# Performance work log

Measured on AMD Instinct MI355X. Metric: run time of the kernel, lower is better.

## Reference

```python
import jax, jax.numpy as jnp
import numpy as np

E = 300      # embedding size
H = 150      # LSTM units per direction
D = 300      # biLSTM output dim (2*H)
VOCAB = 200000
SEQ = 2048


def _lstm(x, W, U, b, reverse=False):
    # x: [S, E] -> hidden states [S, H]; keras gate order i,f,g(c),o
    xp = x @ W + b  # [S, 4H]
    h0 = jnp.zeros((H,), x.dtype)
    c0 = jnp.zeros((H,), x.dtype)

    def step(carry, xt):
        h, c = carry
        z = xt + h @ U
        i = jax.nn.sigmoid(z[:H])
        f = jax.nn.sigmoid(z[H:2 * H])
        g = jnp.tanh(z[2 * H:3 * H])
        o = jax.nn.sigmoid(z[3 * H:])
        c = f * c + i * g
        h = o * jnp.tanh(c)
        return (h, c), h

    _, hs = jax.lax.scan(step, (h0, c0), xp, reverse=reverse)
    return hs


def _primary_attention(out, hidden_states, syn_emb):
    # out: [S, D] projected hidden states; syn_emb: [S, 4, E]
    att = jnp.exp(jnp.einsum('sd,skd->sk', out, syn_emb))      # [S, 4]
    m = jnp.einsum('sk,skd->sd', att, syn_emb)                 # [S, E]
    return jnp.concatenate([hidden_states, m], axis=-1)        # [S, D+E]


def _secondary_attention(h, w, b):
    coeff = jnp.exp(jnp.tanh(h @ w + b))                       # [S, 1]
    return jnp.sum(coeff * h, axis=0)                          # [D+E]


def setup_inputs() -> dict:
    key = jax.random.key(0)
    ks = jax.random.split(key, 20)
    s = 0.05
    inp = {
        'sentence': jax.random.randint(ks[0], (SEQ,), 0, VOCAB),
        'embedding_matrix': jax.random.normal(ks[1], (VOCAB, E), jnp.float32),
        'synonym_indices': jax.random.randint(ks[2], (VOCAB, 4), 0, VOCAB),
        # forward LSTM
        'Wf': jax.random.normal(ks[3], (E, 4 * H), jnp.float32) * s,
        'Uf': jax.random.normal(ks[4], (H, 4 * H), jnp.float32) * s,
        'bf': jnp.zeros((4 * H,), jnp.float32),
        # backward LSTM
        'Wb': jax.random.normal(ks[5], (E, 4 * H), jnp.float32) * s,
        'Ub': jax.random.normal(ks[6], (H, 4 * H), jnp.float32) * s,
        'bb': jnp.zeros((4 * H,), jnp.float32),
        # primary attention dense layers (D -> D)
        'W_pe': jax.random.normal(ks[7], (D, D), jnp.float32) * s,
        'b_pe': jnp.zeros((D,), jnp.float32),
        'W_ps': jax.random.normal(ks[8], (D, D), jnp.float32) * s,
        'b_ps': jnp.zeros((D,), jnp.float32),
        # secondary attention dense layers (D+E -> 1, tanh)
        'w_se': jax.random.normal(ks[9], (D + E, 1), jnp.float32) * s,
        'b_se': jnp.zeros((1,), jnp.float32),
        'w_ss': jax.random.normal(ks[10], (D + E, 1), jnp.float32) * s,
        'b_ss': jnp.zeros((1,), jnp.float32),
        # output layers
        'W_eo': jax.random.normal(ks[11], (D + E, 8), jnp.float32) * s,
        'b_eo': jnp.zeros((8,), jnp.float32),
        'W_so': jax.random.normal(ks[12], (D + E, 1), jnp.float32) * s,
        'b_so': jnp.zeros((1,), jnp.float32),
    }
    return inp


def reference(sentence, embedding_matrix, synonym_indices,
              Wf, Uf, bf, Wb, Ub, bb,
              W_pe, b_pe, W_ps, b_ps,
              w_se, b_se, w_ss, b_ss,
              W_eo, b_eo, W_so, b_so):
    embeddings = embedding_matrix[sentence]                    # [S, E]
    h_fwd = _lstm(embeddings, Wf, Uf, bf, reverse=False)       # [S, H]
    h_bwd = _lstm(embeddings, Wb, Ub, bb, reverse=True)        # [S, H]
    hidden_states = jnp.concatenate([h_fwd, h_bwd], axis=-1)   # [S, D]

    syn_emb = embedding_matrix[synonym_indices[sentence]]      # [S, 4, E]

    out_s = hidden_states @ W_ps + b_ps
    h_hats = _primary_attention(out_s, hidden_states, syn_emb)  # [S, D+E]
    out_e = hidden_states @ W_pe + b_pe
    h_bars = _primary_attention(out_e, hidden_states, syn_emb)  # [S, D+E]

    H_HAT = _secondary_attention(h_hats, w_ss, b_ss)[None, :]   # [1, D+E]
    H_BAR = _secondary_attention(h_bars, w_se, b_se)[None, :]   # [1, D+E]

    sentiment_logits = H_HAT @ W_so + b_so                      # [1, 1]
    emotion_logits = H_BAR @ W_eo + b_eo                        # [1, 8]
    return (emotion_logits, sentiment_logits)
```

## Files before the change

kernel.cpp:

```cpp
#include <hip/hip_runtime.h>
#include <hip/hip_bf16.h>

#define SEQ  2048
#define EDIM 300
#define HDIM 150
#define FH   600
#define DDIM 300
#define DE   600

__device__ __forceinline__ float frcp_(float x) { return __builtin_amdgcn_rcpf(x); }
__device__ __forceinline__ float sigm_(float x) { return frcp_(1.f + __expf(-x)); }
__device__ __forceinline__ float tanh_(float x) { return 1.f - 2.f * frcp_(1.f + __expf(2.f * x)); }

__device__ __forceinline__ float wave_red(float v) {
#pragma unroll
    for (int off = 32; off; off >>= 1) v += __shfl_down(v, off, 64);
    return v;
}

__device__ __forceinline__ float rl_(float v, int l) {
    return __uint_as_float((unsigned)__builtin_amdgcn_readlane(__float_as_uint(v), l));
}

__global__ __launch_bounds__(256) void k_xp(
    const int* __restrict__ sent, const float* __restrict__ emb,
    const float* __restrict__ Wf, const float* __restrict__ bfv,
    const float* __restrict__ Wb, const float* __restrict__ bbv,
    float* __restrict__ xpf, float* __restrict__ xpb)
{
    __shared__ float xs[16][EDIM];
    const int tid = threadIdx.x;
    const int t0  = blockIdx.x * 16;

    for (int i = tid; i < 16 * EDIM; i += 256) {
        int r = i / EDIM, e = i - r * EDIM;
        int row = sent[t0 + r];
        xs[r][e] = emb[(size_t)row * EDIM + e];
    }
    __syncthreads();

    float acc[5][16];
#pragma unroll
    for (int c = 0; c < 5; c++)
#pragma unroll
        for (int r = 0; r < 16; r++) acc[c][r] = 0.f;

    const float* wp[5];
    bool val[5];
#pragma unroll
    for (int c = 0; c < 5; c++) {
        int j = tid + 256 * c;
        val[c] = (j < 1200);
        wp[c] = (j < 600) ? (Wf + j) : (Wb + (j < 1200 ? j - 600 : 0));
    }

    for (int e = 0; e < EDIM; e++) {
        float xr[16];
#pragma unroll
        for (int r = 0; r < 16; r++) xr[r] = xs[r][e];
#pragma unroll
        for (int c = 0; c < 5; c++) {
            if (val[c]) {
                float w = wp[c][(size_t)e * FH];
#pragma unroll
                for (int r = 0; r < 16; r++) acc[c][r] += xr[r] * w;
            }
        }
    }

#pragma unroll
    for (int c = 0; c < 5; c++) {
        int j = tid + 256 * c;
        if (j < 1200) {
            bool isF = (j < 600);
            int jj = isF ? j : j - 600;
            float bias = isF ? bfv[jj] : bbv[jj];
            float* dst = isF ? xpf : xpb;
#pragma unroll
            for (int r = 0; r < 16; r++)
                dst[(size_t)(t0 + r) * FH + jj] = acc[c][r] + bias;
        }
    }
}

__global__ __launch_bounds__(512, 2) void k_lstm(
    const float* __restrict__ Uf, const float* __restrict__ Ub,
    const float* __restrict__ xpf, const float* __restrict__ xpb,
    float* __restrict__ hs)
{
    const int dir = blockIdx.x;
    const float* __restrict__ U  = dir ? Ub : Uf;
    const float* __restrict__ xp = dir ? xpb : xpf;

    __shared__ float zpart[2][4][FH];

    const int tid  = threadIdx.x;
    const int lane = tid & 63;
    const int wv   = tid >> 6;
    const int kg   = wv & 3;
    const int cg   = wv >> 2;
    const int kw0  = kg * 38;

    const bool has5 = (lane < 44);
    int col[5];
#pragma unroll
    for (int g = 0; g < 5; g++) {
        int c = 300 * cg + 64 * g + lane;
        col[g] = (g == 4 && !has5) ? (300 * cg + 299) : c;
    }

    float Ur[5][38];
#pragma unroll
    for (int kk = 0; kk < 38; kk++) {
        const int k   = kw0 + kk;
        const bool kv = (k < HDIM);
        const float* row = U + (size_t)(kv ? k : 0) * FH;
        const float m = kv ? 1.f : 0.f;
#pragma unroll
        for (int g = 0; g < 5; g++)
            Ur[g][kk] = m * row[col[g]];
    }

    const int j  = kw0 + lane;
    const bool gv = (lane < 38) && (j < HDIM);
    float hreg = 0.f, creg = 0.f;

    float xq0 = 0.f, xq1 = 0.f, xq2 = 0.f, xq3 = 0.f;
    if (gv) {
        const float* xrow = xp + (size_t)(dir ? (SEQ - 1) : 0) * FH;
        xq0 = xrow[j];
        xq1 = xrow[HDIM + j];
        xq2 = xrow[2 * HDIM + j];
        xq3 = xrow[3 * HDIM + j];
    }

    for (int step = 0; step < SEQ; step++) {
        const int t = dir ? (SEQ - 1 - step) : step;
        const int p = step & 1;

        float s0 = 0.f, s1 = 0.f, s2 = 0.f, s3 = 0.f, s4 = 0.f;
#pragma unroll
        for (int kk = 0; kk < 38; kk++) {
            const float hk = rl_(hreg, kk);
            s0 = fmaf(hk, Ur[0][kk], s0);
            s1 = fmaf(hk, Ur[1][kk], s1);
            s2 = fmaf(hk, Ur[2][kk], s2);
            s3 = fmaf(hk, Ur[3][kk], s3);
            s4 = fmaf(hk, Ur[4][kk], s4);
        }
        zpart[p][kg][col[0]] = s0;
        zpart[p][kg][col[1]] = s1;
        zpart[p][kg][col[2]] = s2;
        zpart[p][kg][col[3]] = s3;
        if (has5) zpart[p][kg][col[4]] = s4;

        asm volatile("s_waitcnt lgkmcnt(0)" ::: "memory");
        __builtin_amdgcn_sched_barrier(0);
        __builtin_amdgcn_s_barrier();
        __builtin_amdgcn_sched_barrier(0);

        if (gv) {
            float z0 = xq0, z1 = xq1, z2 = xq2, z3 = xq3;
#pragma unroll
            for (int k4 = 0; k4 < 4; k4++) {
                z0 += zpart[p][k4][j];
                z1 += zpart[p][k4][HDIM + j];
                z2 += zpart[p][k4][2 * HDIM + j];
                z3 += zpart[p][k4][3 * HDIM + j];
            }

            if (step + 1 < SEQ) {
                const int tn = dir ? (SEQ - 2 - step) : (step + 1);
                const float* xrow = xp + (size_t)tn * FH;
                xq0 = xrow[j];
                xq1 = xrow[HDIM + j];
                xq2 = xrow[2 * HDIM + j];
                xq3 = xrow[3 * HDIM + j];
            }

            const float ig = sigm_(z0);
            const float fg = sigm_(z1);
            const float gg = tanh_(z2);
            const float og = sigm_(z3);
            creg = fg * creg + ig * gg;
            hreg = og * tanh_(creg);

            if (cg == 0)
                hs[(size_t)t * DDIM + dir * HDIM + j] = hreg;
        }
    }
}

__global__ __launch_bounds__(256) void k_out(
    const float* __restrict__ hs,
    const float* __restrict__ Wpe, const float* __restrict__ bpe,
    const float* __restrict__ Wps, const float* __restrict__ bps,
    float* __restrict__ oe, float* __restrict__ os)
{
    __shared__ float xs[16 * DDIM];
    const int tid = threadIdx.x;
    const int t0  = blockIdx.x * 16;

    for (int i = tid; i < 16 * DDIM; i += 256) xs[i] = hs[(size_t)t0 * DDIM + i];
    __syncthreads();

    float acc[3][16];
#pragma unroll
    for (int c = 0; c < 3; c++)
#pragma unroll
        for (int r = 0; r < 16; r++) acc[c][r] = 0.f;

    const float* wp[3];
    bool val[3];
#pragma unroll
    for (int c = 0; c < 3; c++) {
        int j = tid + 256 * c;
        val[c] = (j < 600);
        wp[c] = (j < 300) ? (Wpe + j) : (Wps + (j < 600 ? j - 300 : 0));
    }

    for (int e = 0; e < DDIM; e++) {
        float xr[16];
#pragma unroll
        for (int r = 0; r < 16; r++) xr[r] = xs[r * DDIM + e];
#pragma unroll
        for (int c = 0; c < 3; c++) {
            if (val[c]) {
                float w = wp[c][(size_t)e * DDIM];
#pragma unroll
                for (int r = 0; r < 16; r++) acc[c][r] += xr[r] * w;
            }
        }
    }

#pragma unroll
    for (int c = 0; c < 3; c++) {
        int j = tid + 256 * c;
        if (j < 600) {
            bool isE = (j < 300);
            int jj = isE ? j : j - 300;
            float bias = isE ? bpe[jj] : bps[jj];
            float* dst = isE ? oe : os;
#pragma unroll
            for (int r = 0; r < 16; r++)
                dst[(size_t)(t0 + r) * DDIM + jj] = acc[c][r] + bias;
        }
    }
}

__global__ __launch_bounds__(256) void k_attn(
    const int* __restrict__ sent, const int* __restrict__ syn,
    const float* __restrict__ emb,
    const float* __restrict__ hs, const float* __restrict__ oeA, const float* __restrict__ osA,
    const float* __restrict__ w_se, const float* __restrict__ b_se,
    const float* __restrict__ w_ss, const float* __restrict__ b_ss,
    float* __restrict__ accHat, float* __restrict__ accBar)
{
    __shared__ float Loe[DDIM], Los[DDIM], Lh[DDIM];
    __shared__ float Lsyn[4][EDIM];
    __shared__ float Lme[EDIM], Lms[EDIM];
    __shared__ float Lred[4][8];
    __shared__ float Latt[8];
    __shared__ float Lco[2];

    const int tid = threadIdx.x;
    const int wv = tid >> 6, lane = tid & 63;
    float aH[3] = {0.f, 0.f, 0.f}, aB[3] = {0.f, 0.f, 0.f};

    for (int i8 = 0; i8 < 8; i8++) {
        const int s = blockIdx.x * 8 + i8;
        for (int i = tid; i < DDIM; i += 256) {
            Loe[i] = oeA[(size_t)s * DDIM + i];
            Los[i] = osA[(size_t)s * DDIM + i];
            Lh[i]  = hs [(size_t)s * DDIM + i];
        }
        const int sid = sent[s];
        for (int i = tid; i < 4 * EDIM; i += 256) {
            int k4 = i / EDIM, e = i - k4 * EDIM;
            int row = syn[sid * 4 + k4];
            Lsyn[k4][e] = emb[(size_t)row * EDIM + e];
        }
        __syncthreads();

        float p[8];
#pragma unroll
        for (int q = 0; q < 8; q++) p[q] = 0.f;
        for (int d = tid; d < EDIM; d += 256) {
            float voe = Loe[d], vos = Los[d];
#pragma unroll
            for (int k4 = 0; k4 < 4; k4++) {
                float sv = Lsyn[k4][d];
                p[k4]     += voe * sv;
                p[4 + k4] += vos * sv;
            }
        }
#pragma unroll
        for (int q = 0; q < 8; q++) {
            float r = wave_red(p[q]);
            if (lane == 0) Lred[wv][q] = r;
        }
        __syncthreads();
        if (tid < 8)
            Latt[tid] = __expf(Lred[0][tid] + Lred[1][tid] + Lred[2][tid] + Lred[3][tid]);
        __syncthreads();

        for (int d = tid; d < EDIM; d += 256) {
            float me = 0.f, ms = 0.f;
#pragma unroll
            for (int k4 = 0; k4 < 4; k4++) {
                float sv = Lsyn[k4][d];
                me += Latt[k4] * sv;
                ms += Latt[4 + k4] * sv;
            }
            Lme[d] = me; Lms[d] = ms;
        }
        __syncthreads();

        float pe = 0.f, ps = 0.f;
        for (int d = tid; d < DE; d += 256) {
            float ve = (d < DDIM) ? Lh[d] : Lme[d - DDIM];
            float vs = (d < DDIM) ? Lh[d] : Lms[d - DDIM];
            pe += ve * w_se[d];
            ps += vs * w_ss[d];
        }
        pe = wave_red(pe); ps = wave_red(ps);
        if (lane == 0) { Lred[wv][0] = pe; Lred[wv][1] = ps; }
        __syncthreads();
        if (tid == 0) {
            float de_ = Lred[0][0] + Lred[1][0] + Lred[2][0] + Lred[3][0];
            float ds_ = Lred[0][1] + Lred[1][1] + Lred[2][1] + Lred[3][1];
            Lco[0] = __expf(tanh_(de_ + b_se[0]));
            Lco[1] = __expf(tanh_(ds_ + b_ss[0]));
        }
        __syncthreads();
        float ce = Lco[0], cs = Lco[1];
#pragma unroll
        for (int cc = 0; cc < 3; cc++) {
            int d = tid + 256 * cc;
            if (d < DE) {
                float ve = (d < DDIM) ? Lh[d] : Lme[d - DDIM];
                float vs = (d < DDIM) ? Lh[d] : Lms[d - DDIM];
                aB[cc] += ce * ve;
                aH[cc] += cs * vs;
            }
        }
        __syncthreads();
    }

#pragma unroll
    for (int cc = 0; cc < 3; cc++) {
        int d = tid + 256 * cc;
        if (d < DE) {
            atomicAdd(&accHat[d], aH[cc]);
            atomicAdd(&accBar[d], aB[cc]);
        }
    }
}

__global__ __launch_bounds__(64) void k_final(
    const float* __restrict__ accHat, const float* __restrict__ accBar,
    const float* __restrict__ W_eo, const float* __restrict__ b_eo,
    const float* __restrict__ W_so, const float* __restrict__ b_so,
    float* __restrict__ out)
{
    const int lane = threadIdx.x;
#pragma unroll
    for (int jq = 0; jq < 8; jq++) {
        float pp = 0.f;
        for (int d = lane; d < DE; d += 64) pp += accBar[d] * W_eo[d * 8 + jq];
        pp = wave_red(pp);
        if (lane == 0) out[jq] = pp + b_eo[jq];
    }
    float pp = 0.f;
    for (int d = lane; d < DE; d += 64) pp += accHat[d] * W_so[d];
    pp = wave_red(pp);
    if (lane == 0) out[8] = pp + b_so[0];
}

extern "C" void kernel_launch(void* const* d_in, const int* in_sizes, int n_in,
                              void* d_out, int out_size, void* d_ws, size_t ws_size,
                              hipStream_t stream)
{
    const int*   sent = (const int*)  d_in[0];
    const float* emb  = (const float*)d_in[1];
    const int*   syn  = (const int*)  d_in[2];
    const float* Wf   = (const float*)d_in[3];
    const float* Uf   = (const float*)d_in[4];
    const float* bfv  = (const float*)d_in[5];
    const float* Wb   = (const float*)d_in[6];
    const float* Ub   = (const float*)d_in[7];
    const float* bbv  = (const float*)d_in[8];
    const float* Wpe  = (const float*)d_in[9];
    const float* bpe  = (const float*)d_in[10];
    const float* Wps  = (const float*)d_in[11];
    const float* bps  = (const float*)d_in[12];
    const float* wse  = (const float*)d_in[13];
    const float* bse  = (const float*)d_in[14];
    const float* wss  = (const float*)d_in[15];
    const float* bss  = (const float*)d_in[16];
    const float* Weo  = (const float*)d_in[17];
    const float* beo  = (const float*)d_in[18];
    const float* Wso  = (const float*)d_in[19];
    const float* bso  = (const float*)d_in[20];

    float* ws  = (float*)d_ws;
    float* xpf = ws;
    float* xpb = xpf + (size_t)SEQ * FH;
    float* hsA = xpb + (size_t)SEQ * FH;
    float* oeA = hsA + (size_t)SEQ * DDIM;
    float* osA = oeA + (size_t)SEQ * DDIM;
    float* accHat = osA + (size_t)SEQ * DDIM;
    float* accBar = accHat + DE;

    hipMemsetAsync(accHat, 0, 2 * DE * sizeof(float), stream);

    k_xp  <<<SEQ / 16, 256, 0, stream>>>(sent, emb, Wf, bfv, Wb, bbv, xpf, xpb);
    k_lstm<<<2,        512, 0, stream>>>(Uf, Ub, xpf, xpb, hsA);
    k_out <<<SEQ / 16, 256, 0, stream>>>(hsA, Wpe, bpe, Wps, bps, oeA, osA);
    k_attn<<<SEQ / 8,  256, 0, stream>>>(sent, syn, emb, hsA, oeA, osA,
                                         wse, bse, wss, bss, accHat, accBar);
    k_final<<<1,        64, 0, stream>>>(accHat, accBar, Weo, beo, Wso, bso,
                                         (float*)d_out);
}
```

Baseline: 3.627 ms.

## Split LSTM recurrence over 16 waves and parallelize gate activations

The recurrent LSTM kernel now runs 1024 threads per direction. The hidden dimension is split into 8 k-groups of 19 rows instead of 4 of 38, which halves the serial readlane/FMA chain per step. Gate nonlinearities are now computed by 600 threads, one per gate element, and stored in shared memory before a second barrier; after that the 150 cell-update lanes combine them. The cost is an extra block-wide barrier per timestep, twice as many partial sums to reduce, removal of the zpart double buffer, and tighter register limits from the larger launch bound.

```diff
diff --git a/kernel.cpp b/kernel.cpp
--- a/kernel.cpp
+++ b/kernel.cpp
@@ -83,7 +83,7 @@
     }
 }
 
-__global__ __launch_bounds__(512, 2) void k_lstm(
+__global__ __launch_bounds__(1024, 4) void k_lstm(
     const float* __restrict__ Uf, const float* __restrict__ Ub,
     const float* __restrict__ xpf, const float* __restrict__ xpb,
     float* __restrict__ hs)
@@ -92,14 +92,15 @@
     const float* __restrict__ U  = dir ? Ub : Uf;
     const float* __restrict__ xp = dir ? xpb : xpf;
 
-    __shared__ float zpart[2][4][FH];
+    __shared__ float zpart[8][FH];
+    __shared__ float act[FH];
 
     const int tid  = threadIdx.x;
     const int lane = tid & 63;
     const int wv   = tid >> 6;
-    const int kg   = wv & 3;
-    const int cg   = wv >> 2;
-    const int kw0  = kg * 38;
+    const int kg   = wv & 7;
+    const int cg   = wv >> 3;
+    const int kw0  = kg * 19;
 
     const bool has5 = (lane < 44);
     int col[5];
@@ -109,9 +110,9 @@
         col[g] = (g == 4 && !has5) ? (300 * cg + 299) : c;
     }
 
-    float Ur[5][38];
-#pragma unroll
-    for (int kk = 0; kk < 38; kk++) {
+    float Ur[5][19];
+#pragma unroll
+    for (int kk = 0; kk < 19; kk++) {
         const int k   = kw0 + kk;
         const bool kv = (k < HDIM);
         const float* row = U + (size_t)(kv ? k : 0) * FH;
@@ -122,25 +123,20 @@
     }
 
     const int j  = kw0 + lane;
-    const bool gv = (lane < 38) && (j < HDIM);
+    const bool gv = (lane < 19) && (j < HDIM);
     float hreg = 0.f, creg = 0.f;
 
-    float xq0 = 0.f, xq1 = 0.f, xq2 = 0.f, xq3 = 0.f;
-    if (gv) {
-        const float* xrow = xp + (size_t)(dir ? (SEQ - 1) : 0) * FH;
-        xq0 = xrow[j];
-        xq1 = xrow[HDIM + j];
-        xq2 = xrow[2 * HDIM + j];
-        xq3 = xrow[3 * HDIM + j];
-    }
+    const bool bv   = (tid < FH);
+    const int  gsel = tid / 150;
+    float xq = 0.f;
+    if (bv) xq = xp[(size_t)(dir ? (SEQ - 1) : 0) * FH + tid];
 
     for (int step = 0; step < SEQ; step++) {
         const int t = dir ? (SEQ - 1 - step) : step;
-        const int p = step & 1;
 
         float s0 = 0.f, s1 = 0.f, s2 = 0.f, s3 = 0.f, s4 = 0.f;
 #pragma unroll
-        for (int kk = 0; kk < 38; kk++) {
+        for (int kk = 0; kk < 19; kk++) {
             const float hk = rl_(hreg, kk);
             s0 = fmaf(hk, Ur[0][kk], s0);
             s1 = fmaf(hk, Ur[1][kk], s1);
@@ -148,43 +144,43 @@
             s3 = fmaf(hk, Ur[3][kk], s3);
             s4 = fmaf(hk, Ur[4][kk], s4);
         }
-        zpart[p][kg][col[0]] = s0;
-        zpart[p][kg][col[1]] = s1;
-        zpart[p][kg][col[2]] = s2;
-        zpart[p][kg][col[3]] = s3;
-        if (has5) zpart[p][kg][col[4]] = s4;
+        zpart[kg][col[0]] = s0;
+        zpart[kg][col[1]] = s1;
+        zpart[kg][col[2]] = s2;
+        zpart[kg][col[3]] = s3;
+        if (has5) zpart[kg][col[4]] = s4;
 
         asm volatile("s_waitcnt lgkmcnt(0)" ::: "memory");
         __builtin_amdgcn_sched_barrier(0);
         __builtin_amdgcn_s_barrier();
         __builtin_amdgcn_sched_barrier(0);
 
-        if (gv) {
-            float z0 = xq0, z1 = xq1, z2 = xq2, z3 = xq3;
-#pragma unroll
-            for (int k4 = 0; k4 < 4; k4++) {
-                z0 += zpart[p][k4][j];
-                z1 += zpart[p][k4][HDIM + j];
-                z2 += zpart[p][k4][2 * HDIM + j];
-                z3 += zpart[p][k4][3 * HDIM + j];
-            }
+        if (bv) {
+            float z = xq;
+#pragma unroll
+            for (int k8 = 0; k8 < 8; k8++)
+                z += zpart[k8][tid];
 
             if (step + 1 < SEQ) {
                 const int tn = dir ? (SEQ - 2 - step) : (step + 1);
-                const float* xrow = xp + (size_t)tn * FH;
-                xq0 = xrow[j];
-                xq1 = xrow[HDIM + j];
-                xq2 = xrow[2 * HDIM + j];
-                xq3 = xrow[3 * HDIM + j];
-            }
-
-            const float ig = sigm_(z0);
-            const float fg = sigm_(z1);
-            const float gg = tanh_(z2);
-            const float og = sigm_(z3);
+                xq = xp[(size_t)tn * FH + tid];
+            }
+
+            act[tid] = (gsel == 2) ? tanh_(z) : sigm_(z);
+        }
+
+        asm volatile("s_waitcnt lgkmcnt(0)" ::: "memory");
+        __builtin_amdgcn_sched_barrier(0);
+        __builtin_amdgcn_s_barrier();
+        __builtin_amdgcn_sched_barrier(0);
+
+        if (gv) {
+            const float ig = act[j];
+            const float fg = act[HDIM + j];
+            const float gg = act[2 * HDIM + j];
+            const float og = act[3 * HDIM + j];
             creg = fg * creg + ig * gg;
             hreg = og * tanh_(creg);
-
             if (cg == 0)
                 hs[(size_t)t * DDIM + dir * HDIM + j] = hreg;
         }
@@ -415,7 +411,7 @@
     hipMemsetAsync(accHat, 0, 2 * DE * sizeof(float), stream);
 
     k_xp  <<<SEQ / 16, 256, 0, stream>>>(sent, emb, Wf, bfv, Wb, bbv, xpf, xpb);
-    k_lstm<<<2,        512, 0, stream>>>(Uf, Ub, xpf, xpb, hsA);
+    k_lstm<<<2,       1024, 0, stream>>>(Uf, Ub, xpf, xpb, hsA);
     k_out <<<SEQ / 16, 256, 0, stream>>>(hsA, Wpe, bpe, Wps, bps, oeA, osA);
     k_attn<<<SEQ / 8,  256, 0, stream>>>(sent, syn, emb, hsA, oeA, osA,
                                          wse, bse, wss, bss, accHat, accBar);
```

Result: no change. 3.693 ms (+1.8%).
